# Performance work log

Hardware: AMD Instinct MI355X
Metric: run time of the kernel (lower is better)

The kernel has to match this reference:

```python
import jax, jax.numpy as jnp
import numpy as np

SLOPE = 0.2  # LeakyReLU negative slope

def _mlp2(x, w1, b1, w2, b2):
    h = jax.nn.leaky_relu(x @ w1 + b1, SLOPE)
    return h @ w2 + b2

def setup_inputs() -> dict:
    key = jax.random.key(0)
    ks = jax.random.split(key, 16)
    B, N, T, A, H = 8, 512, 8, 16, 64
    D = T * A  # node_dim * timestep = 128
    s = 0.1
    return {
        "nodes": jax.random.normal(ks[0], (B, N, T, A), dtype=jnp.float32),
        "edges": jax.random.randint(ks[1], (B, N, N), 0, 2),
        "self_w1": jax.random.normal(ks[2], (D, H), dtype=jnp.float32) * s,
        "self_b1": jnp.zeros((H,), jnp.float32),
        "self_w2": jax.random.normal(ks[3], (H, H), dtype=jnp.float32) * s,
        "self_b2": jnp.zeros((H,), jnp.float32),
        "nb_w1": jax.random.normal(ks[4], (D, H), dtype=jnp.float32) * s,
        "nb_b1": jnp.zeros((H,), jnp.float32),
        "nb_w2": jax.random.normal(ks[5], (H, H), dtype=jnp.float32) * s,
        "nb_b2": jnp.zeros((H,), jnp.float32),
        "comb_w1": jax.random.normal(ks[6], (2 * H, H), dtype=jnp.float32) * s,
        "comb_b1": jnp.zeros((H,), jnp.float32),
        "comb_w2": jax.random.normal(ks[7], (H, 1), dtype=jnp.float32) * s,
        "comb_b2": jnp.zeros((1,), jnp.float32),
    }

def reference(nodes, edges, self_w1, self_b1, self_w2, self_b2,
              nb_w1, nb_b1, nb_w2, nb_b2,
              comb_w1, comb_b1, comb_w2, comb_b2):
    B, N = nodes.shape[0], nodes.shape[1]
    H = self_w2.shape[1]
    x = nodes.reshape(B, N, -1)                       # [B,N,D]
    self_e = _mlp2(x, self_w1, self_b1, self_w2, self_b2)  # [B,N,H]
    nb_e = _mlp2(x, nb_w1, nb_b1, nb_w2, nb_b2)            # [B,N,H]

    # combine_mlp(cat(self_i, nb_j)) scores; split fc1 to avoid [B,N,N,2H]
    w1_s, w1_n = comb_w1[:H], comb_w1[H:]
    pre = (jnp.einsum('bih,hk->bik', self_e, w1_s)[:, :, None, :]
           + jnp.einsum('bjh,hk->bjk', nb_e, w1_n)[:, None, :, :]
           + comb_b1)                                  # [B,N,N,H] (i=target, j=neighbor)
    scores = (jax.nn.leaky_relu(pre, SLOPE) @ comb_w2)[..., 0] + comb_b2[0]  # [B,N,N]

    # mask[b,i,j] = edges[b,j,i] != 0 and i != j
    mask = (jnp.swapaxes(edges, 1, 2) != 0) & (~jnp.eye(N, dtype=bool))
    neg = jnp.finfo(scores.dtype).min
    weights = jax.nn.softmax(jnp.where(mask, scores, neg), axis=-1)
    weights = jnp.where(mask, weights, 0.0)

    agg = jnp.einsum('bij,bjh->bih', weights, nb_e)    # weighted neighbor sum
    has_nb = mask.any(-1)                              # nodes w/o neighbors stay zero
    return jnp.where(has_nb[..., None], agg + self_e, 0.0)
```

## Files before the change

### kernel.cpp

```cpp
#include <hip/hip_runtime.h>
#include <float.h>

typedef __attribute__((ext_vector_type(8))) short short8;
typedef __attribute__((ext_vector_type(4))) float f32x4;

#define SLOPE 0.2f

__device__ __forceinline__ float leaky(float x) { return fmaxf(x, SLOPE * x); }

__device__ __forceinline__ unsigned short f2bf(float f) {
  unsigned u = __float_as_uint(f);
  return (unsigned short)((u + 0x7FFFu + ((u >> 16) & 1u)) >> 16);
}

__global__ __launch_bounds__(256) void node_mlps(
    const float* __restrict__ nodes,
    const float* __restrict__ self_w1, const float* __restrict__ self_b1,
    const float* __restrict__ self_w2, const float* __restrict__ self_b2,
    const float* __restrict__ nb_w1,   const float* __restrict__ nb_b1,
    const float* __restrict__ nb_w2,   const float* __restrict__ nb_b2,
    const float* __restrict__ comb_w1, const float* __restrict__ comb_b1,
    const float* __restrict__ comb_w2, const float* __restrict__ comb_b2,
    float* __restrict__ self_e,
    float* __restrict__ ss, float* __restrict__ sn,
    float* __restrict__ sP, float* __restrict__ sQ,
    unsigned short* __restrict__ nbT)
{
  __shared__ float x_sh[8][128];
  __shared__ float h_sh[8][64];
  __shared__ float e_sh[8][64];

  const int tid = threadIdx.x, lane = tid & 63, wv = tid >> 6;
  const int node0 = blockIdx.x * 8;
  const int bb = node0 >> 9;
  const int jloc = node0 & 511;

  ((float4*)&x_sh[0][0])[tid] = ((const float4*)(nodes + (size_t)node0 * 128))[tid];
  __syncthreads();

  const int la = wv * 2, lb = la + 1;
  const float w2lane = comb_w2[lane];
  const float cb2 = comb_b2[0];
  const float cb1 = comb_b1[lane];

  for (int p = 0; p < 2; ++p) {
    const float* w1 = p ? nb_w1 : self_w1;
    const float* b1 = p ? nb_b1 : self_b1;
    const float* w2 = p ? nb_w2 : self_w2;
    const float* b2 = p ? nb_b2 : self_b2;
    const float* cw = comb_w1 + (p ? 64 * 64 : 0);

    float a0 = 0.f, a1 = 0.f, c0 = 0.f, c1 = 0.f;
    #pragma unroll 4
    for (int q = 0; q < 32; ++q) {
      float4 xa = *(const float4*)&x_sh[la][q * 4];
      float4 xb = *(const float4*)&x_sh[lb][q * 4];
      float w_0 = w1[(q * 4 + 0) * 64 + lane];
      float w_1 = w1[(q * 4 + 1) * 64 + lane];
      float w_2 = w1[(q * 4 + 2) * 64 + lane];
      float w_3 = w1[(q * 4 + 3) * 64 + lane];
      a0 += xa.x * w_0; a1 += xa.y * w_1; a0 += xa.z * w_2; a1 += xa.w * w_3;
      c0 += xb.x * w_0; c1 += xb.y * w_1; c0 += xb.z * w_2; c1 += xb.w * w_3;
    }
    {
      float bv = b1[lane];
      h_sh[la][lane] = leaky(a0 + a1 + bv);
      h_sh[lb][lane] = leaky(c0 + c1 + bv);
    }
    __syncthreads();

    a0 = a1 = c0 = c1 = 0.f;
    #pragma unroll 4
    for (int q = 0; q < 16; ++q) {
      float4 ha = *(const float4*)&h_sh[la][q * 4];
      float4 hb = *(const float4*)&h_sh[lb][q * 4];
      float w_0 = w2[(q * 4 + 0) * 64 + lane];
      float w_1 = w2[(q * 4 + 1) * 64 + lane];
      float w_2 = w2[(q * 4 + 2) * 64 + lane];
      float w_3 = w2[(q * 4 + 3) * 64 + lane];
      a0 += ha.x * w_0; a1 += ha.y * w_1; a0 += ha.z * w_2; a1 += ha.w * w_3;
      c0 += hb.x * w_0; c1 += hb.y * w_1; c0 += hb.z * w_2; c1 += hb.w * w_3;
    }
    float e_a, e_b;
    {
      float bv = b2[lane];
      e_a = a0 + a1 + bv;
      e_b = c0 + c1 + bv;
    }
    e_sh[la][lane] = e_a;
    e_sh[lb][lane] = e_b;
    if (p == 0) {
      self_e[(size_t)(node0 + la) * 64 + lane] = e_a;
      self_e[(size_t)(node0 + lb) * 64 + lane] = e_b;
    }
    __syncthreads();

    a0 = a1 = c0 = c1 = 0.f;
    #pragma unroll 4
    for (int q = 0; q < 16; ++q) {
      float4 ea = *(const float4*)&e_sh[la][q * 4];
      float4 eb = *(const float4*)&e_sh[lb][q * 4];
      float w_0 = cw[(q * 4 + 0) * 64 + lane];
      float w_1 = cw[(q * 4 + 1) * 64 + lane];
      float w_2 = cw[(q * 4 + 2) * 64 + lane];
      float w_3 = cw[(q * 4 + 3) * 64 + lane];
      a0 += ea.x * w_0; a1 += ea.y * w_1; a0 += ea.z * w_2; a1 += ea.w * w_3;
      c0 += eb.x * w_0; c1 += eb.y * w_1; c0 += eb.z * w_2; c1 += eb.w * w_3;
    }
    float s_a = a0 + a1 + (p ? 0.f : cb1);
    float s_b = c0 + c1 + (p ? 0.f : cb1);
    {
      float* so = p ? sn : ss;
      so[(size_t)(node0 + la) * 64 + lane] = s_a;
      so[(size_t)(node0 + lb) * 64 + lane] = s_b;
    }
    float ra = w2lane * s_a, rb = w2lane * s_b;
    #pragma unroll
    for (int off = 32; off; off >>= 1) {
      ra += __shfl_xor(ra, off);
      rb += __shfl_xor(rb, off);
    }
    if (lane == 0) {
      float* po = p ? sQ : sP;
      float add = p ? 0.f : cb2;
      po[node0 + la] = 0.6f * ra + add;
      po[node0 + lb] = 0.6f * rb + add;
    }

    if (p == 1) {
      float v0 = e_sh[la][lane];
      float v1 = e_sh[lb][lane];
      unsigned pack = (unsigned)f2bf(v0) | ((unsigned)f2bf(v1) << 16);
      *(unsigned*)(nbT + ((size_t)(bb * 64 + lane) * 512 + jloc + la)) = pack;
    }
    __syncthreads();
  }
}

__global__ __launch_bounds__(512) void gat_attn(
    const int* __restrict__ edges,
    const float* __restrict__ comb_w2,
    const float* __restrict__ self_e,
    const float* __restrict__ ss, const float* __restrict__ sn,
    const float* __restrict__ sP, const float* __restrict__ sQ,
    const unsigned short* __restrict__ nbT,
    float* __restrict__ out)
{
  __shared__ __align__(16) float sn_sh[2][64][68];
  __shared__ __align__(16) unsigned short P_sh[16][520];
  __shared__ __align__(16) float red_sh[4][64][4];
  __shared__ float f_sh[16];

  const int tid = threadIdx.x, lane = tid & 63, wv = tid >> 6;
  const int b = blockIdx.x & 7, it = blockIdx.x >> 3;
  const int i0 = it * 16;
  const size_t nodeb = (size_t)b * 512;

  const int ra = wv * 2, rb = ra + 1;
  const int ia = i0 + ra, ib = ia + 1;

  unsigned em0 = 0, em1 = 0;
  float sQv[8];
  #pragma unroll
  for (int jt = 0; jt < 8; ++jt) {
    const int j = jt * 64 + lane;
    int2 e2 = *(const int2*)&edges[((size_t)(nodeb + j)) * 512 + ia];
    sQv[jt] = sQ[nodeb + j];
    em0 |= (e2.x != 0 ? 1u : 0u) << jt;
    em1 |= (e2.y != 0 ? 1u : 0u) << jt;
  }
  {
    const int d0 = ia - lane;
    if (d0 >= 0 && (d0 & 63) == 0) em0 &= ~(1u << (d0 >> 6));
    const int d1 = ib - lane;
    if (d1 >= 0 && (d1 & 63) == 0) em1 &= ~(1u << (d1 >> 6));
  }

  float4 w2p[16], sa0[16], sa1[16];
  {
    const float4* w2v = (const float4*)comb_w2;
    const float4* s0 = (const float4*)(ss + (nodeb + ia) * 64);
    const float4* s1 = (const float4*)(ss + (nodeb + ib) * 64);
    #pragma unroll
    for (int q = 0; q < 16; ++q) {
      float4 w = w2v[q];
      w2p[q] = make_float4(0.4f * w.x, 0.4f * w.y, 0.4f * w.z, 0.4f * w.w);
      sa0[q] = s0[q];
      sa1[q] = s1[q];
    }
  }
  const float sPa = sP[nodeb + ia], sPb = sP[nodeb + ib];

  const int str = tid >> 4, stc = (tid & 15) * 4;
  const int str2 = (tid + 512) >> 4, stc2 = ((tid + 512) & 15) * 4;
  float4 st0, st1;
  {
    const float4* src = (const float4*)(sn + nodeb * 64);
    st0 = src[tid];
    st1 = src[tid + 512];
  }

  float msc0[8], msc1[8];
  int cur = 0;
  for (int jt = 0; jt < 8; ++jt) {
    *(float4*)&sn_sh[cur][str][stc] = st0;
    *(float4*)&sn_sh[cur][str2][stc2] = st1;
    if (jt < 7) {
      const float4* src = (const float4*)(sn + (nodeb + (jt + 1) * 64) * 64);
      st0 = src[tid];
      st1 = src[tid + 512];
    }
    __syncthreads();

    float acc0 = 0.f, acc1 = 0.f;
    #pragma unroll
    for (int q = 0; q < 16; ++q) {
      float4 v = *(const float4*)&sn_sh[cur][lane][q * 4];
      float4 w = w2p[q];
      float4 A = sa0[q];
      float4 Bv = sa1[q];
      acc0 += w.x * fabsf(A.x + v.x) + w.y * fabsf(A.y + v.y)
            + w.z * fabsf(A.z + v.z) + w.w * fabsf(A.w + v.w);
      acc1 += w.x * fabsf(Bv.x + v.x) + w.y * fabsf(Bv.y + v.y)
            + w.z * fabsf(Bv.z + v.z) + w.w * fabsf(Bv.w + v.w);
    }
    msc0[jt] = ((em0 >> jt) & 1u) ? acc0 + sPa + sQv[jt] : -FLT_MAX;
    msc1[jt] = ((em1 >> jt) & 1u) ? acc1 + sPb + sQv[jt] : -FLT_MAX;
    cur ^= 1;
  }

  float m0 = msc0[0], m1 = msc1[0];
  #pragma unroll
  for (int jt = 1; jt < 8; ++jt) {
    m0 = fmaxf(m0, msc0[jt]);
    m1 = fmaxf(m1, msc1[jt]);
  }
  #pragma unroll
  for (int off = 32; off; off >>= 1) {
    m0 = fmaxf(m0, __shfl_xor(m0, off));
    m1 = fmaxf(m1, __shfl_xor(m1, off));
  }

  float s0 = 0.f, s1 = 0.f;
  #pragma unroll
  for (int jt = 0; jt < 8; ++jt) {
    const float e0 = __expf(msc0[jt] - m0);
    const float e1 = __expf(msc1[jt] - m1);
    P_sh[ra][jt * 64 + lane] = f2bf(e0);
    P_sh[rb][jt * 64 + lane] = f2bf(e1);
    s0 += e0;
    s1 += e1;
  }
  #pragma unroll
  for (int off = 32; off; off >>= 1) {
    s0 += __shfl_xor(s0, off);
    s1 += __shfl_xor(s1, off);
  }
  if (lane == 0) {
    f_sh[ra] = (m0 > -1e37f) ? 1.0f / s0 : 0.0f;
    f_sh[rb] = (m1 > -1e37f) ? 1.0f / s1 : 0.0f;
  }
  __syncthreads();

  const int nt = wv & 3, kh = wv >> 2;
  const int arow = lane & 15, agrp = lane >> 4;
  const int bcol = nt * 16 + (lane & 15);
  const unsigned short* nbrow = nbT + ((size_t)(b * 64 + bcol)) * 512;

  f32x4 C = {0.f, 0.f, 0.f, 0.f};
  #pragma unroll
  for (int ks = 0; ks < 8; ++ks) {
    const int jb = kh * 256 + ks * 32 + agrp * 8;
    short8 afr = *(const short8*)&P_sh[arow][jb];
    short8 bfr = *(const short8*)(nbrow + jb);
    C = __builtin_amdgcn_mfma_f32_16x16x32_bf16(afr, bfr, C, 0, 0, 0);
  }
  if (kh == 1) *(f32x4*)&red_sh[wv - 4][lane][0] = C;
  __syncthreads();
  if (kh == 0) {
    f32x4 P = *(const f32x4*)&red_sh[wv][lane][0];
    #pragma unroll
    for (int r = 0; r < 4; ++r) {
      const int rg = agrp * 4 + r;
      const float f = f_sh[rg];
      const size_t adr = (nodeb + i0 + rg) * 64 + bcol;
      const float val = (C[r] + P[r]) * f + self_e[adr];
      out[adr] = (f > 0.f) ? val : 0.f;
    }
  }
}

extern "C" void kernel_launch(void* const* d_in, const int* in_sizes, int n_in,
                              void* d_out, int out_size, void* d_ws, size_t ws_size,
                              hipStream_t stream) {
  const float* nodes   = (const float*)d_in[0];
  const int*   edges   = (const int*)  d_in[1];
  const float* self_w1 = (const float*)d_in[2];
  const float* self_b1 = (const float*)d_in[3];
  const float* self_w2 = (const float*)d_in[4];
  const float* self_b2 = (const float*)d_in[5];
  const float* nb_w1   = (const float*)d_in[6];
  const float* nb_b1   = (const float*)d_in[7];
  const float* nb_w2   = (const float*)d_in[8];
  const float* nb_b2   = (const float*)d_in[9];
  const float* comb_w1 = (const float*)d_in[10];
  const float* comb_b1 = (const float*)d_in[11];
  const float* comb_w2 = (const float*)d_in[12];
  const float* comb_b2 = (const float*)d_in[13];

  float* ws     = (float*)d_ws;
  float* self_e = ws;
  float* ss     = ws + 262144;
  float* sn     = ws + 524288;
  float* sP     = ws + 786432;
  float* sQ     = ws + 790528;
  unsigned short* nbT = (unsigned short*)(ws + 794624);

  node_mlps<<<512, 256, 0, stream>>>(
      nodes, self_w1, self_b1, self_w2, self_b2,
      nb_w1, nb_b1, nb_w2, nb_b2, comb_w1, comb_b1, comb_w2, comb_b2,
      self_e, ss, sn, sP, sQ, nbT);

  gat_attn<<<256, 512, 0, stream>>>(
      edges, comb_w2, self_e, ss, sn, sP, sQ, nbT, (float*)d_out);
}
```

Baseline: 38.86 us.

## Pack edge mask into bitmasks in prep kernel and retile node MLPs

The first kernel gains extra blocks that read the int32 edge matrix with coalesced tile loads, transpose it through shared memory and write 64-bit ballot bitmasks per target node. The attention kernel then reads these compact bitmasks instead of doing strided int2 gathers across the edge matrix. The node MLP part is retiled to 16 nodes per block with 4 nodes per thread, reusing each weight load across more nodes. The cost is an extra workspace buffer and the mask transpose running inside the first kernel, which the attention kernel must wait for.

```diff
diff --git a/kernel.cpp b/kernel.cpp
--- a/kernel.cpp
+++ b/kernel.cpp
@@ -13,35 +13,69 @@
   return (unsigned short)((u + 0x7FFFu + ((u >> 16) & 1u)) >> 16);
 }
 
-__global__ __launch_bounds__(256) void node_mlps(
-    const float* __restrict__ nodes,
+__global__ __launch_bounds__(256) void prep(
+    const float* __restrict__ nodes, const int* __restrict__ edges,
     const float* __restrict__ self_w1, const float* __restrict__ self_b1,
     const float* __restrict__ self_w2, const float* __restrict__ self_b2,
     const float* __restrict__ nb_w1,   const float* __restrict__ nb_b1,
     const float* __restrict__ nb_w2,   const float* __restrict__ nb_b2,
     const float* __restrict__ comb_w1, const float* __restrict__ comb_b1,
     const float* __restrict__ comb_w2, const float* __restrict__ comb_b2,
-    float* __restrict__ self_e,
-    float* __restrict__ ss, float* __restrict__ sn,
+    float* __restrict__ self_e, float* __restrict__ ss, float* __restrict__ sn,
     float* __restrict__ sP, float* __restrict__ sQ,
-    unsigned short* __restrict__ nbT)
+    unsigned short* __restrict__ nbT, unsigned long long* __restrict__ ep)
 {
-  __shared__ float x_sh[8][128];
-  __shared__ float h_sh[8][64];
-  __shared__ float e_sh[8][64];
+  __shared__ float x_sh[16][132];
+  __shared__ float h_sh[16][68];
+  __shared__ float e_sh[16][68];
+  __shared__ float s_sh[16][68];
+  __shared__ int   t_sh[64][65];
 
   const int tid = threadIdx.x, lane = tid & 63, wv = tid >> 6;
-  const int node0 = blockIdx.x * 8;
+
+  if (blockIdx.x >= 256) {
+    const int blk = blockIdx.x - 256;
+    const int b = blk >> 3, it = blk & 7;
+    const int i0 = it * 64;
+    for (int jt = 0; jt < 8; ++jt) {
+      #pragma unroll
+      for (int r = 0; r < 4; ++r) {
+        const int idx = r * 256 + tid;
+        const int jr = idx >> 4, i4 = (idx & 15) * 4;
+        *(int4*)&t_sh[jr][i4] =
+            *(const int4*)&edges[((size_t)(b * 512 + jt * 64 + jr)) * 512 + i0 + i4];
+      }
+      __syncthreads();
+      #pragma unroll
+      for (int u = 0; u < 16; ++u) {
+        const int ic = wv * 16 + u;
+        const unsigned long long m = __ballot(t_sh[lane][ic] != 0);
+        if (lane == 0) ep[((size_t)(b * 512 + i0 + ic)) * 8 + jt] = m;
+      }
+      __syncthreads();
+    }
+    return;
+  }
+
+  const int node0 = blockIdx.x * 16;
   const int bb = node0 >> 9;
   const int jloc = node0 & 511;
 
-  ((float4*)&x_sh[0][0])[tid] = ((const float4*)(nodes + (size_t)node0 * 128))[tid];
+  {
+    const float4* src = (const float4*)(nodes + (size_t)node0 * 128);
+    #pragma unroll
+    for (int r = 0; r < 2; ++r) {
+      const int idx = r * 256 + tid;
+      const int row = idx >> 5, c4 = (idx & 31) * 4;
+      *(float4*)&x_sh[row][c4] = src[idx];
+    }
+  }
   __syncthreads();
 
-  const int la = wv * 2, lb = la + 1;
+  const int c0 = wv * 16 + (lane & 15);
+  const int nd = lane >> 4;
   const float w2lane = comb_w2[lane];
   const float cb2 = comb_b2[0];
-  const float cb1 = comb_b1[lane];
 
   for (int p = 0; p < 2; ++p) {
     const float* w1 = p ? nb_w1 : self_w1;
@@ -50,95 +84,103 @@
     const float* b2 = p ? nb_b2 : self_b2;
     const float* cw = comb_w1 + (p ? 64 * 64 : 0);
 
-    float a0 = 0.f, a1 = 0.f, c0 = 0.f, c1 = 0.f;
+    float acc[4];
+    {
+      const float bv = b1[c0];
+      #pragma unroll
+      for (int u = 0; u < 4; ++u) acc[u] = bv;
+    }
     #pragma unroll 4
     for (int q = 0; q < 32; ++q) {
-      float4 xa = *(const float4*)&x_sh[la][q * 4];
-      float4 xb = *(const float4*)&x_sh[lb][q * 4];
-      float w_0 = w1[(q * 4 + 0) * 64 + lane];
-      float w_1 = w1[(q * 4 + 1) * 64 + lane];
-      float w_2 = w1[(q * 4 + 2) * 64 + lane];
-      float w_3 = w1[(q * 4 + 3) * 64 + lane];
-      a0 += xa.x * w_0; a1 += xa.y * w_1; a0 += xa.z * w_2; a1 += xa.w * w_3;
-      c0 += xb.x * w_0; c1 += xb.y * w_1; c0 += xb.z * w_2; c1 += xb.w * w_3;
-    }
+      const float w_0 = w1[(q * 4 + 0) * 64 + c0];
+      const float w_1 = w1[(q * 4 + 1) * 64 + c0];
+      const float w_2 = w1[(q * 4 + 2) * 64 + c0];
+      const float w_3 = w1[(q * 4 + 3) * 64 + c0];
+      #pragma unroll
+      for (int u = 0; u < 4; ++u) {
+        const float4 xv = *(const float4*)&x_sh[u * 4 + nd][q * 4];
+        acc[u] += xv.x * w_0 + xv.y * w_1 + xv.z * w_2 + xv.w * w_3;
+      }
+    }
+    #pragma unroll
+    for (int u = 0; u < 4; ++u) h_sh[u * 4 + nd][c0] = leaky(acc[u]);
+    __syncthreads();
+
     {
-      float bv = b1[lane];
-      h_sh[la][lane] = leaky(a0 + a1 + bv);
-      h_sh[lb][lane] = leaky(c0 + c1 + bv);
-    }
-    __syncthreads();
-
-    a0 = a1 = c0 = c1 = 0.f;
+      const float bv = b2[c0];
+      #pragma unroll
+      for (int u = 0; u < 4; ++u) acc[u] = bv;
+    }
     #pragma unroll 4
     for (int q = 0; q < 16; ++q) {
-      float4 ha = *(const float4*)&h_sh[la][q * 4];
-      float4 hb = *(const float4*)&h_sh[lb][q * 4];
-      float w_0 = w2[(q * 4 + 0) * 64 + lane];
-      float w_1 = w2[(q * 4 + 1) * 64 + lane];
-      float w_2 = w2[(q * 4 + 2) * 64 + lane];
-      float w_3 = w2[(q * 4 + 3) * 64 + lane];
-      a0 += ha.x * w_0; a1 += ha.y * w_1; a0 += ha.z * w_2; a1 += ha.w * w_3;
-      c0 += hb.x * w_0; c1 += hb.y * w_1; c0 += hb.z * w_2; c1 += hb.w * w_3;
-    }
-    float e_a, e_b;
+      const float w_0 = w2[(q * 4 + 0) * 64 + c0];
+      const float w_1 = w2[(q * 4 + 1) * 64 + c0];
+      const float w_2 = w2[(q * 4 + 2) * 64 + c0];
+      const float w_3 = w2[(q * 4 + 3) * 64 + c0];
+      #pragma unroll
+      for (int u = 0; u < 4; ++u) {
+        const float4 hv = *(const float4*)&h_sh[u * 4 + nd][q * 4];
+        acc[u] += hv.x * w_0 + hv.y * w_1 + hv.z * w_2 + hv.w * w_3;
+      }
+    }
+    #pragma unroll
+    for (int u = 0; u < 4; ++u) {
+      e_sh[u * 4 + nd][c0] = acc[u];
+      if (p == 0) self_e[(size_t)(node0 + u * 4 + nd) * 64 + c0] = acc[u];
+    }
+    __syncthreads();
+
     {
-      float bv = b2[lane];
-      e_a = a0 + a1 + bv;
-      e_b = c0 + c1 + bv;
-    }
-    e_sh[la][lane] = e_a;
-    e_sh[lb][lane] = e_b;
-    if (p == 0) {
-      self_e[(size_t)(node0 + la) * 64 + lane] = e_a;
-      self_e[(size_t)(node0 + lb) * 64 + lane] = e_b;
-    }
-    __syncthreads();
-
-    a0 = a1 = c0 = c1 = 0.f;
+      const float bv = p ? 0.f : comb_b1[c0];
+      #pragma unroll
+      for (int u = 0; u < 4; ++u) acc[u] = bv;
+    }
     #pragma unroll 4
     for (int q = 0; q < 16; ++q) {
-      float4 ea = *(const float4*)&e_sh[la][q * 4];
-      float4 eb = *(const float4*)&e_sh[lb][q * 4];
-      float w_0 = cw[(q * 4 + 0) * 64 + lane];
-      float w_1 = cw[(q * 4 + 1) * 64 + lane];
-      float w_2 = cw[(q * 4 + 2) * 64 + lane];
-      float w_3 = cw[(q * 4 + 3) * 64 + lane];
-      a0 += ea.x * w_0; a1 += ea.y * w_1; a0 += ea.z * w_2; a1 += ea.w * w_3;
-      c0 += eb.x * w_0; c1 += eb.y * w_1; c0 += eb.z * w_2; c1 += eb.w * w_3;
-    }
-    float s_a = a0 + a1 + (p ? 0.f : cb1);
-    float s_b = c0 + c1 + (p ? 0.f : cb1);
+      const float w_0 = cw[(q * 4 + 0) * 64 + c0];
+      const float w_1 = cw[(q * 4 + 1) * 64 + c0];
+      const float w_2 = cw[(q * 4 + 2) * 64 + c0];
+      const float w_3 = cw[(q * 4 + 3) * 64 + c0];
+      #pragma unroll
+      for (int u = 0; u < 4; ++u) {
+        const float4 ev = *(const float4*)&e_sh[u * 4 + nd][q * 4];
+        acc[u] += ev.x * w_0 + ev.y * w_1 + ev.z * w_2 + ev.w * w_3;
+      }
+    }
     {
       float* so = p ? sn : ss;
-      so[(size_t)(node0 + la) * 64 + lane] = s_a;
-      so[(size_t)(node0 + lb) * 64 + lane] = s_b;
-    }
-    float ra = w2lane * s_a, rb = w2lane * s_b;
-    #pragma unroll
-    for (int off = 32; off; off >>= 1) {
-      ra += __shfl_xor(ra, off);
-      rb += __shfl_xor(rb, off);
-    }
-    if (lane == 0) {
-      float* po = p ? sQ : sP;
-      float add = p ? 0.f : cb2;
-      po[node0 + la] = 0.6f * ra + add;
-      po[node0 + lb] = 0.6f * rb + add;
-    }
-
+      #pragma unroll
+      for (int u = 0; u < 4; ++u) {
+        s_sh[u * 4 + nd][c0] = acc[u];
+        so[(size_t)(node0 + u * 4 + nd) * 64 + c0] = acc[u];
+      }
+    }
+    __syncthreads();
+
+    #pragma unroll
+    for (int u = 0; u < 4; ++u) {
+      float r = s_sh[wv * 4 + u][lane] * w2lane;
+      #pragma unroll
+      for (int off = 32; off; off >>= 1) r += __shfl_xor(r, off);
+      if (lane == 0) {
+        float* po = p ? sQ : sP;
+        po[node0 + wv * 4 + u] = 0.6f * r + (p ? 0.f : cb2);
+      }
+    }
     if (p == 1) {
-      float v0 = e_sh[la][lane];
-      float v1 = e_sh[lb][lane];
-      unsigned pack = (unsigned)f2bf(v0) | ((unsigned)f2bf(v1) << 16);
-      *(unsigned*)(nbT + ((size_t)(bb * 64 + lane) * 512 + jloc + la)) = pack;
+      unsigned short v0 = f2bf(e_sh[wv * 4 + 0][lane]);
+      unsigned short v1 = f2bf(e_sh[wv * 4 + 1][lane]);
+      unsigned short v2 = f2bf(e_sh[wv * 4 + 2][lane]);
+      unsigned short v3 = f2bf(e_sh[wv * 4 + 3][lane]);
+      *(ushort4*)(nbT + ((size_t)(bb * 64 + lane)) * 512 + jloc + wv * 4) =
+          make_ushort4(v0, v1, v2, v3);
     }
     __syncthreads();
   }
 }
 
 __global__ __launch_bounds__(512) void gat_attn(
-    const int* __restrict__ edges,
+    const unsigned long long* __restrict__ ep,
     const float* __restrict__ comb_w2,
     const float* __restrict__ self_e,
     const float* __restrict__ ss, const float* __restrict__ sn,
@@ -161,13 +203,15 @@
 
   unsigned em0 = 0, em1 = 0;
   float sQv[8];
-  #pragma unroll
-  for (int jt = 0; jt < 8; ++jt) {
-    const int j = jt * 64 + lane;
-    int2 e2 = *(const int2*)&edges[((size_t)(nodeb + j)) * 512 + ia];
-    sQv[jt] = sQ[nodeb + j];
-    em0 |= (e2.x != 0 ? 1u : 0u) << jt;
-    em1 |= (e2.y != 0 ? 1u : 0u) << jt;
+  {
+    const unsigned long long* e0 = ep + (nodeb + ia) * 8;
+    const unsigned long long* e1 = ep + (nodeb + ib) * 8;
+    #pragma unroll
+    for (int jt = 0; jt < 8; ++jt) {
+      em0 |= (unsigned)((e0[jt] >> lane) & 1ull) << jt;
+      em1 |= (unsigned)((e1[jt] >> lane) & 1ull) << jt;
+      sQv[jt] = sQ[nodeb + jt * 64 + lane];
+    }
   }
   {
     const int d0 = ia - lane;
@@ -315,12 +359,13 @@
   float* sP     = ws + 786432;
   float* sQ     = ws + 790528;
   unsigned short* nbT = (unsigned short*)(ws + 794624);
-
-  node_mlps<<<512, 256, 0, stream>>>(
-      nodes, self_w1, self_b1, self_w2, self_b2,
+  unsigned long long* ep = (unsigned long long*)(ws + 925696);
+
+  prep<<<320, 256, 0, stream>>>(
+      nodes, edges, self_w1, self_b1, self_w2, self_b2,
       nb_w1, nb_b1, nb_w2, nb_b2, comb_w1, comb_b1, comb_w2, comb_b2,
-      self_e, ss, sn, sP, sQ, nbT);
+      self_e, ss, sn, sP, sQ, nbT, ep);
 
   gat_attn<<<256, 512, 0, stream>>>(
-      edges, comb_w2, self_e, ss, sn, sP, sQ, nbT, (float*)d_out);
+      ep, comb_w2, self_e, ss, sn, sP, sQ, nbT, (float*)d_out);
 }
```

Result: slower. 51.40 us (+32.3%).

## Pre-pack transposed edge mask into bitmasks in extra prep blocks

Applied to the files above, without the earlier changes.

Adds 64 extra blocks to the node MLP kernel. They read the edge matrix with coalesced int4 loads, transpose it through shared memory, and ballot it into 64-bit neighbor bitmasks. The attention kernel then reads these compact bitmasks instead of doing strided int2 loads of the full edge matrix. The bf16 packing of nb embeddings now uses register values rather than rereading shared memory. This costs an extra workspace buffer, and the large shared tile may reduce occupancy of the MLP blocks.

```diff
diff --git a/kernel.cpp b/kernel.cpp
--- a/kernel.cpp
+++ b/kernel.cpp
@@ -13,24 +13,49 @@
   return (unsigned short)((u + 0x7FFFu + ((u >> 16) & 1u)) >> 16);
 }
 
-__global__ __launch_bounds__(256) void node_mlps(
-    const float* __restrict__ nodes,
+__global__ __launch_bounds__(256) void prep(
+    const float* __restrict__ nodes, const int* __restrict__ edges,
     const float* __restrict__ self_w1, const float* __restrict__ self_b1,
     const float* __restrict__ self_w2, const float* __restrict__ self_b2,
     const float* __restrict__ nb_w1,   const float* __restrict__ nb_b1,
     const float* __restrict__ nb_w2,   const float* __restrict__ nb_b2,
     const float* __restrict__ comb_w1, const float* __restrict__ comb_b1,
     const float* __restrict__ comb_w2, const float* __restrict__ comb_b2,
-    float* __restrict__ self_e,
-    float* __restrict__ ss, float* __restrict__ sn,
+    float* __restrict__ self_e, float* __restrict__ ss, float* __restrict__ sn,
     float* __restrict__ sP, float* __restrict__ sQ,
-    unsigned short* __restrict__ nbT)
+    unsigned short* __restrict__ nbT, unsigned long long* __restrict__ ep)
 {
   __shared__ float x_sh[8][128];
   __shared__ float h_sh[8][64];
   __shared__ float e_sh[8][64];
+  __shared__ int   t_sh[64][65];
 
   const int tid = threadIdx.x, lane = tid & 63, wv = tid >> 6;
+
+  if (blockIdx.x >= 512) {
+    const int blk = blockIdx.x - 512;
+    const int b = blk >> 3, it = blk & 7;
+    const int i0 = it * 64;
+    for (int jt = 0; jt < 8; ++jt) {
+      #pragma unroll
+      for (int r = 0; r < 4; ++r) {
+        const int idx = r * 256 + tid;
+        const int jr = idx >> 4, i4 = (idx & 15) * 4;
+        *(int4*)&t_sh[jr][i4] =
+            *(const int4*)&edges[((size_t)(b * 512 + jt * 64 + jr)) * 512 + i0 + i4];
+      }
+      __syncthreads();
+      #pragma unroll
+      for (int u = 0; u < 16; ++u) {
+        const int ic = wv * 16 + u;
+        const unsigned long long m = __ballot(t_sh[lane][ic] != 0);
+        if (lane == 0) ep[((size_t)(b * 512 + i0 + ic)) * 8 + jt] = m;
+      }
+      __syncthreads();
+    }
+    return;
+  }
+
   const int node0 = blockIdx.x * 8;
   const int bb = node0 >> 9;
   const int jloc = node0 & 511;
@@ -128,9 +153,7 @@
     }
 
     if (p == 1) {
-      float v0 = e_sh[la][lane];
-      float v1 = e_sh[lb][lane];
-      unsigned pack = (unsigned)f2bf(v0) | ((unsigned)f2bf(v1) << 16);
+      unsigned pack = (unsigned)f2bf(e_a) | ((unsigned)f2bf(e_b) << 16);
       *(unsigned*)(nbT + ((size_t)(bb * 64 + lane) * 512 + jloc + la)) = pack;
     }
     __syncthreads();
@@ -138,7 +161,7 @@
 }
 
 __global__ __launch_bounds__(512) void gat_attn(
-    const int* __restrict__ edges,
+    const unsigned long long* __restrict__ ep,
     const float* __restrict__ comb_w2,
     const float* __restrict__ self_e,
     const float* __restrict__ ss, const float* __restrict__ sn,
@@ -161,13 +184,15 @@
 
   unsigned em0 = 0, em1 = 0;
   float sQv[8];
-  #pragma unroll
-  for (int jt = 0; jt < 8; ++jt) {
-    const int j = jt * 64 + lane;
-    int2 e2 = *(const int2*)&edges[((size_t)(nodeb + j)) * 512 + ia];
-    sQv[jt] = sQ[nodeb + j];
-    em0 |= (e2.x != 0 ? 1u : 0u) << jt;
-    em1 |= (e2.y != 0 ? 1u : 0u) << jt;
+  {
+    const unsigned long long* e0 = ep + (nodeb + ia) * 8;
+    const unsigned long long* e1 = ep + (nodeb + ib) * 8;
+    #pragma unroll
+    for (int jt = 0; jt < 8; ++jt) {
+      em0 |= (unsigned)((e0[jt] >> lane) & 1ull) << jt;
+      em1 |= (unsigned)((e1[jt] >> lane) & 1ull) << jt;
+      sQv[jt] = sQ[nodeb + jt * 64 + lane];
+    }
   }
   {
     const int d0 = ia - lane;
@@ -315,12 +340,13 @@
   float* sP     = ws + 786432;
   float* sQ     = ws + 790528;
   unsigned short* nbT = (unsigned short*)(ws + 794624);
-
-  node_mlps<<<512, 256, 0, stream>>>(
-      nodes, self_w1, self_b1, self_w2, self_b2,
+  unsigned long long* ep = (unsigned long long*)(ws + 925696);
+
+  prep<<<576, 256, 0, stream>>>(
+      nodes, edges, self_w1, self_b1, self_w2, self_b2,
       nb_w1, nb_b1, nb_w2, nb_b2, comb_w1, comb_b1, comb_w2, comb_b2,
-      self_e, ss, sn, sP, sQ, nbT);
+      self_e, ss, sn, sP, sQ, nbT, ep);
 
   gat_attn<<<256, 512, 0, stream>>>(
-      edges, comb_w2, self_e, ss, sn, sP, sQ, nbT, (float*)d_out);
+      ep, comb_w2, self_e, ss, sn, sP, sQ, nbT, (float*)d_out);
 }
```

Result: slower. 42.26 us (+8.7%).

## Coalesce edge mask loads, block nbT layout, drop wave-local barriers

Applied to the files above, without the earlier changes.

The attention kernel now has each thread read 16 contiguous edge entries for one source node with int4 loads. It packs them into a 16-bit mask in shared memory, instead of issuing scattered int2 loads per lane. The neighbor-embedding transpose nbT is stored in a blocked [batch][j/8][h][8] layout, so the prep kernel writes it coalesced after one barrier, and the MFMA B-fragment loads use the new strides. Barriers between stages whose shared rows are only touched by the same wave are removed. These changes aim to cut uncoalesced global traffic and synchronization, at the cost of an extra shared-memory mask array and stride-64 fragment reads.

```diff
diff --git a/kernel.cpp b/kernel.cpp
--- a/kernel.cpp
+++ b/kernel.cpp
@@ -13,7 +13,7 @@
   return (unsigned short)((u + 0x7FFFu + ((u >> 16) & 1u)) >> 16);
 }
 
-__global__ __launch_bounds__(256) void node_mlps(
+__global__ __launch_bounds__(256) void prep(
     const float* __restrict__ nodes,
     const float* __restrict__ self_w1, const float* __restrict__ self_b1,
     const float* __restrict__ self_w2, const float* __restrict__ self_b2,
@@ -21,8 +21,7 @@
     const float* __restrict__ nb_w2,   const float* __restrict__ nb_b2,
     const float* __restrict__ comb_w1, const float* __restrict__ comb_b1,
     const float* __restrict__ comb_w2, const float* __restrict__ comb_b2,
-    float* __restrict__ self_e,
-    float* __restrict__ ss, float* __restrict__ sn,
+    float* __restrict__ self_e, float* __restrict__ ss, float* __restrict__ sn,
     float* __restrict__ sP, float* __restrict__ sQ,
     unsigned short* __restrict__ nbT)
 {
@@ -67,7 +66,6 @@
       h_sh[la][lane] = leaky(a0 + a1 + bv);
       h_sh[lb][lane] = leaky(c0 + c1 + bv);
     }
-    __syncthreads();
 
     a0 = a1 = c0 = c1 = 0.f;
     #pragma unroll 4
@@ -93,7 +91,6 @@
       self_e[(size_t)(node0 + la) * 64 + lane] = e_a;
       self_e[(size_t)(node0 + lb) * 64 + lane] = e_b;
     }
-    __syncthreads();
 
     a0 = a1 = c0 = c1 = 0.f;
     #pragma unroll 4
@@ -128,12 +125,12 @@
     }
 
     if (p == 1) {
-      float v0 = e_sh[la][lane];
-      float v1 = e_sh[lb][lane];
-      unsigned pack = (unsigned)f2bf(v0) | ((unsigned)f2bf(v1) << 16);
-      *(unsigned*)(nbT + ((size_t)(bb * 64 + lane) * 512 + jloc + la)) = pack;
-    }
-    __syncthreads();
+      __syncthreads();
+      const int h = tid >> 2, j2 = (tid & 3) * 2;
+      unsigned pack = (unsigned)f2bf(e_sh[j2][h])
+                    | ((unsigned)f2bf(e_sh[j2 + 1][h]) << 16);
+      *(unsigned*)(nbT + ((size_t)(bb * 64 + (jloc >> 3))) * 512 + h * 8 + j2) = pack;
+    }
   }
 }
 
@@ -149,6 +146,7 @@
   __shared__ __align__(16) float sn_sh[2][64][68];
   __shared__ __align__(16) unsigned short P_sh[16][520];
   __shared__ __align__(16) float red_sh[4][64][4];
+  __shared__ unsigned short jm_sh[512];
   __shared__ float f_sh[16];
 
   const int tid = threadIdx.x, lane = tid & 63, wv = tid >> 6;
@@ -159,22 +157,11 @@
   const int ra = wv * 2, rb = ra + 1;
   const int ia = i0 + ra, ib = ia + 1;
 
-  unsigned em0 = 0, em1 = 0;
-  float sQv[8];
-  #pragma unroll
-  for (int jt = 0; jt < 8; ++jt) {
-    const int j = jt * 64 + lane;
-    int2 e2 = *(const int2*)&edges[((size_t)(nodeb + j)) * 512 + ia];
-    sQv[jt] = sQ[nodeb + j];
-    em0 |= (e2.x != 0 ? 1u : 0u) << jt;
-    em1 |= (e2.y != 0 ? 1u : 0u) << jt;
-  }
-  {
-    const int d0 = ia - lane;
-    if (d0 >= 0 && (d0 & 63) == 0) em0 &= ~(1u << (d0 >> 6));
-    const int d1 = ib - lane;
-    if (d1 >= 0 && (d1 & 63) == 0) em1 &= ~(1u << (d1 >> 6));
-  }
+  const int* eb = edges + ((size_t)(nodeb + tid)) * 512 + i0;
+  const int4 ev0 = *(const int4*)(eb + 0);
+  const int4 ev1 = *(const int4*)(eb + 4);
+  const int4 ev2 = *(const int4*)(eb + 8);
+  const int4 ev3 = *(const int4*)(eb + 12);
 
   float4 w2p[16], sa0[16], sa1[16];
   {
@@ -190,6 +177,24 @@
     }
   }
   const float sPa = sP[nodeb + ia], sPb = sP[nodeb + ib];
+  float sQv[8];
+  #pragma unroll
+  for (int jt = 0; jt < 8; ++jt) sQv[jt] = sQ[nodeb + jt * 64 + lane];
+
+  {
+    unsigned mj = 0;
+    mj |= (ev0.x != 0 ? 1u : 0u) << 0;  mj |= (ev0.y != 0 ? 1u : 0u) << 1;
+    mj |= (ev0.z != 0 ? 1u : 0u) << 2;  mj |= (ev0.w != 0 ? 1u : 0u) << 3;
+    mj |= (ev1.x != 0 ? 1u : 0u) << 4;  mj |= (ev1.y != 0 ? 1u : 0u) << 5;
+    mj |= (ev1.z != 0 ? 1u : 0u) << 6;  mj |= (ev1.w != 0 ? 1u : 0u) << 7;
+    mj |= (ev2.x != 0 ? 1u : 0u) << 8;  mj |= (ev2.y != 0 ? 1u : 0u) << 9;
+    mj |= (ev2.z != 0 ? 1u : 0u) << 10; mj |= (ev2.w != 0 ? 1u : 0u) << 11;
+    mj |= (ev3.x != 0 ? 1u : 0u) << 12; mj |= (ev3.y != 0 ? 1u : 0u) << 13;
+    mj |= (ev3.z != 0 ? 1u : 0u) << 14; mj |= (ev3.w != 0 ? 1u : 0u) << 15;
+    const int d = tid - i0;
+    if (d >= 0 && d < 16) mj &= ~(1u << d);
+    jm_sh[tid] = (unsigned short)mj;
+  }
 
   const int str = tid >> 4, stc = (tid & 15) * 4;
   const int str2 = (tid + 512) >> 4, stc2 = ((tid + 512) & 15) * 4;
@@ -224,8 +229,9 @@
       acc1 += w.x * fabsf(Bv.x + v.x) + w.y * fabsf(Bv.y + v.y)
             + w.z * fabsf(Bv.z + v.z) + w.w * fabsf(Bv.w + v.w);
     }
-    msc0[jt] = ((em0 >> jt) & 1u) ? acc0 + sPa + sQv[jt] : -FLT_MAX;
-    msc1[jt] = ((em1 >> jt) & 1u) ? acc1 + sPb + sQv[jt] : -FLT_MAX;
+    const unsigned mj = jm_sh[jt * 64 + lane];
+    msc0[jt] = ((mj >> ra) & 1u) ? acc0 + sPa + sQv[jt] : -FLT_MAX;
+    msc1[jt] = ((mj >> rb) & 1u) ? acc1 + sPb + sQv[jt] : -FLT_MAX;
     cur ^= 1;
   }
 
@@ -265,14 +271,14 @@
   const int nt = wv & 3, kh = wv >> 2;
   const int arow = lane & 15, agrp = lane >> 4;
   const int bcol = nt * 16 + (lane & 15);
-  const unsigned short* nbrow = nbT + ((size_t)(b * 64 + bcol)) * 512;
+  const unsigned short* nb3 = nbT + (size_t)b * 32768 + bcol * 8;
 
   f32x4 C = {0.f, 0.f, 0.f, 0.f};
   #pragma unroll
   for (int ks = 0; ks < 8; ++ks) {
     const int jb = kh * 256 + ks * 32 + agrp * 8;
     short8 afr = *(const short8*)&P_sh[arow][jb];
-    short8 bfr = *(const short8*)(nbrow + jb);
+    short8 bfr = *(const short8*)(nb3 + (size_t)jb * 64);
     C = __builtin_amdgcn_mfma_f32_16x16x32_bf16(afr, bfr, C, 0, 0, 0);
   }
   if (kh == 1) *(f32x4*)&red_sh[wv - 4][lane][0] = C;
@@ -316,7 +322,7 @@
   float* sQ     = ws + 790528;
   unsigned short* nbT = (unsigned short*)(ws + 794624);
 
-  node_mlps<<<512, 256, 0, stream>>>(
+  prep<<<512, 256, 0, stream>>>(
       nodes, self_w1, self_b1, self_w2, self_b2,
       nb_w1, nb_b1, nb_w2, nb_b2, comb_w1, comb_b1, comb_w2, comb_b2,
       self_e, ss, sn, sP, sQ, nbT);
```

Measured after the change: 35.79 us. 7.9% less time.
